# Optimization experiments

Measured on AMD Instinct MI355X. Metric: run time of the kernel, lower is better.

## Reference

```python
import jax, jax.numpy as jnp
import numpy as np
from functools import partial

DM, DP, DV = 128, 32, 32
DO = DP + DV
SCALE_F = 4.0
MAXF = 127.0 / SCALE_F                       # 31.75 feature clamp
SCALE_FM = SCALE_F / 16.0 * 3600.0 / 256.0   # scale after spatial mean
MAXM = 127.0 / SCALE_FM                      # clamp after mean
DN = ('NCHW', 'OIHW', 'NCHW')

# 3-tap positions inside a 3x3 kernel for the 4 directions
_DIR_POS = [
    [(1, 0), (1, 1), (1, 2)],  # horizontal
    [(0, 1), (1, 1), (2, 1)],  # vertical
    [(0, 0), (1, 1), (2, 2)],  # main diagonal
    [(2, 0), (1, 1), (0, 2)],  # anti diagonal
]

def _dir_conv(x, w, b, d):
    # w: [3, out, in] -> dense [out, in, 3, 3] kernel with 3 nonzero taps
    o, i = w.shape[1], w.shape[2]
    k = jnp.zeros((o, i, 3, 3), w.dtype)
    for t, (r, c) in enumerate(_DIR_POS[d]):
        k = k.at[:, :, r, c].set(w[t])
    y = jax.lax.conv_general_dilated(x, k, (1, 1), 'SAME', dimension_numbers=DN)
    return y + b[None, :, None, None]

def _pw(x, w, b):  # 1x1 conv: w [out, in]
    return jnp.einsum('bchw,oc->bohw', x, w) + b[None, :, None, None]

def _lrelu16(x):
    return jnp.where(x >= 0, x, x * (1.0 / 16.0))

def forward(x, map_w, map_b, dconv_w, dconv_b, c1_w, c1_b,
            r0_w1, r0_b1, r0_w2, r0_b2, fin_w, fin_b, prelu_w,
            pdw_w, pdw_b, ppw_w, vl1_w, vl1_b, vl2_w, vl2_b,
            vlf_w, vlf_b, pscale, vscale):
    silu = jax.nn.silu
    # ---- Mapping ----
    xs = tuple(silu(_dir_conv(x, map_w, map_b, d)) for d in range(4))
    for l in range(4):  # 4 DirectionalConvResBlocks
        res = xs
        xs = tuple(silu(_dir_conv(xs[d], dconv_w[l], dconv_b[l], d)) for d in range(4))
        xs = tuple(silu(_pw(t, c1_w[l], c1_b[l])) for t in xs)
        xs = tuple(a + b for a, b in zip(xs, res))
    # Conv0dResBlock
    res = xs
    xs = tuple(silu(_pw(t, r0_w1, r0_b1)) for t in xs)
    xs = tuple(silu(_pw(t, r0_w2, r0_b2)) for t in xs)
    xs = tuple(a + b for a, b in zip(xs, res))
    xs = tuple(_pw(t, fin_w, fin_b) for t in xs)
    feature = jnp.stack(xs, axis=1)  # [B, 4, DO, H, W]
    # ---- trunk post-processing ----
    feature = jnp.tanh(feature / MAXF) * MAXF
    feature = jnp.sum(feature, axis=1)  # [B, DO, H, W]
    a = prelu_w[None, :, None, None]
    feature = jnp.where(feature >= 0, feature, a * feature)  # PReLU per-channel
    feature = feature / 4.0
    # ---- policy head ----
    policy = feature[:, :DP]
    policy = jax.lax.conv_general_dilated(policy, pdw_w, (1, 1), 'SAME',
                                          dimension_numbers=DN,
                                          feature_group_count=DP)
    policy = _lrelu16(policy + pdw_b[None, :, None, None])
    policy = jnp.clip(policy, -MAXF, MAXF)
    policy = _lrelu16(jnp.einsum('bchw,oc->bohw', policy, ppw_w))
    policy = policy * pscale
    # ---- value head ----
    value = jnp.mean(feature[:, DP:], axis=(2, 3))  # [B, DV]
    value = jax.nn.relu(value)
    value = jax.nn.relu(value @ vl1_w.T + vl1_b)
    value = jnp.minimum(value, MAXM)
    value = jax.nn.relu(value @ vl2_w.T + vl2_b)
    value = jnp.minimum(value, MAXM)
    value = (value @ vlf_w.T + vlf_b) * vscale
    return (value, policy)

def setup_inputs() -> dict:
    key = jax.random.key(0)
    ks = iter(jax.random.split(key, 32))
    n = lambda shape, s=0.1: (jax.random.normal(next(ks), shape, jnp.float32) * s)
    B, H, W = 512, 15, 15
    return {
        'x': jax.random.uniform(next(ks), (B, 2, H, W), jnp.float32),
        'map_w': n((3, DM, 2), 0.5), 'map_b': jnp.zeros((DM,), jnp.float32),
        'dconv_w': n((4, 3, DM, DM)), 'dconv_b': jnp.zeros((4, DM), jnp.float32),
        'c1_w': n((4, DM, DM)), 'c1_b': jnp.zeros((4, DM), jnp.float32),
        'r0_w1': n((DM, DM)), 'r0_b1': jnp.zeros((DM,), jnp.float32),
        'r0_w2': n((DM, DM)), 'r0_b2': jnp.zeros((DM,), jnp.float32),
        'fin_w': n((DO, DM)), 'fin_b': jnp.zeros((DO,), jnp.float32),
        'prelu_w': jnp.full((DO,), 0.25, jnp.float32),
        'pdw_w': n((DP, 1, 3, 3), 0.3), 'pdw_b': jnp.zeros((DP,), jnp.float32),
        'ppw_w': n((1, DP), 0.3),
        'vl1_w': n((DV, DV), 0.2), 'vl1_b': jnp.zeros((DV,), jnp.float32),
        'vl2_w': n((DV, DV), 0.2), 'vl2_b': jnp.zeros((DV,), jnp.float32),
        'vlf_w': n((3, DV), 0.2), 'vlf_b': jnp.zeros((3,), jnp.float32),
        'pscale': jnp.ones((1,), jnp.float32),
        'vscale': jnp.ones((1,), jnp.float32),
    }

def reference(x, map_w, map_b, dconv_w, dconv_b, c1_w, c1_b,
              r0_w1, r0_b1, r0_w2, r0_b2, fin_w, fin_b, prelu_w,
              pdw_w, pdw_b, ppw_w, vl1_w, vl1_b, vl2_w, vl2_b,
              vlf_w, vlf_b, pscale, vscale):
    return forward(x, map_w, map_b, dconv_w, dconv_b, c1_w, c1_b,
                   r0_w1, r0_b1, r0_w2, r0_b2, fin_w, fin_b, prelu_w,
                   pdw_w, pdw_b, ppw_w, vl1_w, vl1_b, vl2_w, vl2_b,
                   vlf_w, vlf_b, pscale, vscale)
```

## Files before the change

### kernel.cpp

```cpp
#include <hip/hip_runtime.h>
#include <math.h>

typedef unsigned short u16;
typedef _Float16 f16;
typedef __attribute__((ext_vector_type(4))) _Float16 f16x4;
typedef __attribute__((ext_vector_type(8))) _Float16 f16x8;
typedef __attribute__((ext_vector_type(4))) float f32x4;

#define NCELL 225
#define AST   136
#define NROW  227
#define MAXF  31.75f
#define MAXM  (127.0f/((4.0f/16.0f)*3600.0f/256.0f))
#define DYN_LDS (2*NROW*AST*2)

#define W_DCONV 0
#define W_C1    196608
#define W_R01   262144
#define W_R02   278528
#define W_FIN   294912
#define W_F16TOT 303104
#define F_MAPB   0
#define F_DCONVB 128
#define F_C1B    640
#define F_R0B1   1152
#define F_R0B2   1280
#define F_FINB   1408
#define F_PRELU  1472
#define F_MAPW   1536
#define F_TOT    2304

__device__ __forceinline__ float bfu(unsigned h){ union{unsigned i; float f;} v; v.i=h<<16; return v.f; }
__device__ __forceinline__ float rcp_f(float x){ return __builtin_amdgcn_rcpf(x); }
__device__ __forceinline__ float silu_f(float x){ return x*rcp_f(1.f+__expf(-x)); }
__device__ __forceinline__ float tanh_f(float z){ return 1.f - 2.f*rcp_f(__expf(2.f*z)+1.f); }
__device__ __forceinline__ float ldp(const void* p, size_t i, int isf){
  return isf ? ((const float*)p)[i] : bfu(((const u16*)p)[i]);
}

__global__ __launch_bounds__(256) void k_prep(
    const void* __restrict__ dconv_w, const void* __restrict__ c1_w,
    const void* __restrict__ r0_w1,  const void* __restrict__ r0_w2,
    const void* __restrict__ fin_w,  const void* __restrict__ map_w,
    const void* __restrict__ map_b,  const void* __restrict__ dconv_b,
    const void* __restrict__ c1_b,   const void* __restrict__ r0_b1,
    const void* __restrict__ r0_b2,  const void* __restrict__ fin_b,
    const void* __restrict__ prelu_w,
    const void* __restrict__ x, f16* __restrict__ wbuf)
{
  __shared__ int sflag;
  if (threadIdx.x < 64) {
    unsigned v = ((const u16*)x)[2*threadIdx.x];
    unsigned long long m = __ballot(v > 0x4000u);
    if (threadIdx.x == 0) sflag = (__popcll(m) > 16) ? 1 : 0;
  }
  __syncthreads();
  const int isf = sflag;
  float* fsec = (float*)(wbuf + W_F16TOT);
  const int NTOT = W_F16TOT + F_TOT;
  for (int i = blockIdx.x*256 + threadIdx.x; i < NTOT; i += gridDim.x*256) {
    if (i < W_F16TOT) {
      float v; int j = i;
      if (j < 196608)                 v = ldp(dconv_w, j, isf);
      else if ((j -= 196608) < 65536) v = ldp(c1_w, j, isf);
      else if ((j -= 65536) < 16384)  v = ldp(r0_w1, j, isf);
      else if ((j -= 16384) < 16384)  v = ldp(r0_w2, j, isf);
      else { j -= 16384;              v = ldp(fin_w, j, isf); }
      wbuf[i] = (f16)v;
    } else {
      int j = i - W_F16TOT; float v;
      if (j < 128)               v = ldp(map_b, j, isf);
      else if ((j -= 128) < 512) v = ldp(dconv_b, j, isf);
      else if ((j -= 512) < 512) v = ldp(c1_b, j, isf);
      else if ((j -= 512) < 128) v = ldp(r0_b1, j, isf);
      else if ((j -= 128) < 128) v = ldp(r0_b2, j, isf);
      else if ((j -= 128) < 64)  v = ldp(fin_b, j, isf);
      else if ((j -= 64) < 64)   v = ldp(prelu_w, j, isf);
      else { j -= 64;            v = ldp(map_w, j, isf); }
      fsec[i - W_F16TOT] = v;
    }
  }
}

template<int NTAPS, int MODE>
__device__ __forceinline__ void phase(
    const f16* __restrict__ S, f16* __restrict__ D,
    const f16* __restrict__ W, const float* __restrict__ bp,
    const unsigned (&pk)[4], int tid)
{
  const int lane = tid & 63;
  const int lrow = lane & 15;
  const int qb   = lane & 48;
  const int wave = tid >> 6;
  const int cg = wave >> 2, ng = wave & 3;
  const int ch0  = ng*32 + (qb >> 2);
  const int wrow = (ng*32 + lrow)*128 + (qb >> 1);

  f32x4 acc[4][2];
#pragma unroll
  for (int mi = 0; mi < 4; ++mi) {
    f32x4 z = {0.f,0.f,0.f,0.f};
    acc[mi][0] = z; acc[mi][1] = z;
  }
#pragma unroll
  for (int t = 0; t < NTAPS; ++t) {
    const int tt = (NTAPS == 3) ? t : 1;
    const f16* Wt = W + ((NTAPS == 3) ? t*16384 : 0) + wrow;
#pragma clang loop unroll(disable)
    for (int kb = 0; kb < 4; ++kb) {
      f16x8 Wf0 = *(const f16x8*)(Wt + kb*32);
      f16x8 Wf1 = *(const f16x8*)(Wt + 2048 + kb*32);
      f16x8 Af[4];
#pragma unroll
      for (int mi = 0; mi < 4; ++mi) {
        const int pc = (pk[mi] >> (8*tt)) & 255u;
        Af[mi] = *(const f16x8*)((const char*)S + pc*(AST*2) + qb + kb*64);
      }
#pragma unroll
      for (int mi = 0; mi < 4; ++mi) {
        acc[mi][0] = __builtin_amdgcn_mfma_f32_16x16x32_f16(Wf0, Af[mi], acc[mi][0], 0, 0, 0);
        acc[mi][1] = __builtin_amdgcn_mfma_f32_16x16x32_f16(Wf1, Af[mi], acc[mi][1], 0, 0, 0);
      }
    }
  }
  f32x4 bb0 = *(const f32x4*)(bp + ch0);
  f32x4 bb1 = *(const f32x4*)(bp + ch0 + 16);
#pragma unroll
  for (int mi = 0; mi < 4; ++mi) {
    const int cell = (cg*4 + mi)*16 + lrow;
    const int row  = (cell < NCELL) ? cell : 226;
#pragma unroll
    for (int nt = 0; nt < 2; ++nt) {
      f16* dp = D + row*AST + ch0 + nt*16;
      const f32x4 bb = nt ? bb1 : bb0;
      float v0 = silu_f(acc[mi][nt][0] + bb[0]);
      float v1 = silu_f(acc[mi][nt][1] + bb[1]);
      float v2 = silu_f(acc[mi][nt][2] + bb[2]);
      float v3 = silu_f(acc[mi][nt][3] + bb[3]);
      if (MODE == 1) {
        f16x4 r = *(const f16x4*)dp;
        v0 += (float)r[0]; v1 += (float)r[1]; v2 += (float)r[2]; v3 += (float)r[3];
      }
      f16x4 o = { (f16)v0, (f16)v1, (f16)v2, (f16)v3 };
      *(f16x4*)dp = o;
    }
  }
  __syncthreads();
}

__global__ __attribute__((amdgpu_flat_work_group_size(1024, 1024), amdgpu_waves_per_eu(4, 4)))
void k_all(
    const void* __restrict__ x,
    const void* __restrict__ pdw_w,  const void* __restrict__ pdw_b,
    const void* __restrict__ ppw_w,
    const void* __restrict__ vl1_w,  const void* __restrict__ vl1_b,
    const void* __restrict__ vl2_w,  const void* __restrict__ vl2_b,
    const void* __restrict__ vlf_w,  const void* __restrict__ vlf_b,
    const void* __restrict__ pscale, const void* __restrict__ vscale,
    const f16* __restrict__ wbuf, float* __restrict__ out, int badflag)
{
  extern __shared__ __align__(16) char dyn[];
  f16* bufA = (f16*)dyn;
  f16* bufB = bufA + NROW*AST;
  __shared__ float xin[452];
  __shared__ float vred[1024];
  __shared__ float vvA[32], vvB[32];
  __shared__ int sflag;

  const int b = blockIdx.x, tid = threadIdx.x;
  const int lane = tid & 63, wave = tid >> 6;
  const int cg = wave >> 2, ng = wave & 3;
  const int lrow = lane & 15;
  const float* fsec = (const float*)(wbuf + W_F16TOT);

  if (tid < 64) {
    unsigned v = ((const u16*)x)[2*tid];
    unsigned long long m = __ballot(v > 0x4000u);
    if (tid == 0) sflag = (__popcll(m) > 16) ? 1 : 0;
  }
  for (int i = tid; i < AST; i += 1024) {
    bufA[225*AST + i] = (f16)0.f;
    bufB[225*AST + i] = (f16)0.f;
  }
  __syncthreads();
  const int isf = sflag;

  for (int i = tid; i < 452; i += 1024) {
    float v;
    if (i < 225)       v = ldp(x, (size_t)b*450 + i, isf);
    else if (i == 225) v = 0.f;
    else if (i < 451)  v = ldp(x, (size_t)b*450 + 225 + (i - 226), isf);
    else               v = 0.f;
    xin[i] = v;
  }

  float facc[4][2][2];
#pragma unroll
  for (int mi = 0; mi < 4; ++mi)
#pragma unroll
    for (int jp = 0; jp < 2; ++jp) { facc[mi][jp][0] = 0.f; facc[mi][jp][1] = 0.f; }

  __syncthreads();

#pragma clang loop unroll(disable)
  for (int d = 0; d < 4; ++d) {
    const int dr = (d == 0) ? 0 : ((d == 3) ? -1 : 1);
    const int dc = (d == 1) ? 0 : 1;

    unsigned pk[4];
#pragma unroll
    for (int mi = 0; mi < 4; ++mi) {
      const int cell = (cg*4 + mi)*16 + lrow;
      const bool v0 = cell < NCELL;
      const int r = cell/15, c = cell - (cell/15)*15;
      unsigned p = 0;
#pragma unroll
      for (int t = 0; t < 3; ++t) {
        const int rs = r + (t-1)*dr, cs = c + (t-1)*dc;
        const bool v = v0 & (rs >= 0) & (rs < 15) & (cs >= 0) & (cs < 15);
        p |= (unsigned)(v ? rs*15 + cs : 225) << (8*t);
      }
      pk[mi] = p;
    }

    {
      const int qb = lane & 48;
      const int ch0 = ng*32 + (qb >> 2);
      float x0[4][3], x1[4][3];
#pragma unroll
      for (int mi = 0; mi < 4; ++mi)
#pragma unroll
        for (int t = 0; t < 3; ++t) {
          const int sp = (pk[mi] >> (8*t)) & 255u;
          x0[mi][t] = xin[sp]; x1[mi][t] = xin[226 + sp];
        }
#pragma unroll
      for (int nt = 0; nt < 2; ++nt) {
        const int chn = ch0 + nt*16;
        f32x4 mb = *(const f32x4*)(fsec + F_MAPB + chn);
        f32x4 wt[3][2];
#pragma unroll
        for (int t = 0; t < 3; ++t) {
          wt[t][0] = *(const f32x4*)(fsec + F_MAPW + (t*128 + chn)*2);
          wt[t][1] = *(const f32x4*)(fsec + F_MAPW + (t*128 + chn)*2 + 4);
        }
#pragma unroll
        for (int mi = 0; mi < 4; ++mi) {
          const int cell = (cg*4 + mi)*16 + lrow;
          const int row  = (cell < NCELL) ? cell : 226;
          f16x4 o;
#pragma unroll
          for (int j = 0; j < 4; ++j) {
            float s = mb[j];
#pragma unroll
            for (int t = 0; t < 3; ++t)
              s += wt[t][j>>1][(j&1)*2]*x0[mi][t] + wt[t][j>>1][(j&1)*2+1]*x1[mi][t];
            o[j] = (f16)silu_f(s);
          }
          *(f16x4*)(bufA + row*AST + chn) = o;
        }
      }
    }
    __syncthreads();

#pragma clang loop unroll(disable)
    for (int l = 0; l < 4; ++l) {
      phase<3, 0>(bufA, bufB, wbuf + W_DCONV + (size_t)l*49152,
                  fsec + F_DCONVB + l*128, pk, tid);
      phase<1, 1>(bufB, bufA, wbuf + W_C1 + (size_t)l*16384,
                  fsec + F_C1B + l*128, pk, tid);
    }
    phase<1, 0>(bufA, bufB, wbuf + W_R01, fsec + F_R0B1, pk, tid);
    phase<1, 1>(bufB, bufA, wbuf + W_R02, fsec + F_R0B2, pk, tid);

    {
      const int qb = lane & 48;
      f32x4 fa[4];
#pragma unroll
      for (int mi = 0; mi < 4; ++mi) { f32x4 z = {0.f,0.f,0.f,0.f}; fa[mi] = z; }
      const f16* Wt = wbuf + W_FIN + (ng*16 + lrow)*128 + (qb >> 1);
#pragma clang loop unroll(disable)
      for (int kb = 0; kb < 4; ++kb) {
        f16x8 Wf = *(const f16x8*)(Wt + kb*32);
#pragma unroll
        for (int mi = 0; mi < 4; ++mi) {
          const int pc = (pk[mi] >> 8) & 255u;
          f16x8 a = *(const f16x8*)((const char*)bufA + pc*(AST*2) + qb + kb*64);
          fa[mi] = __builtin_amdgcn_mfma_f32_16x16x32_f16(Wf, a, fa[mi], 0, 0, 0);
        }
      }
      const int chf = ng*16 + (qb >> 2);
      f32x4 fb = *(const f32x4*)(fsec + F_FINB + chf);
#pragma unroll
      for (int mi = 0; mi < 4; ++mi)
#pragma unroll
        for (int j = 0; j < 4; ++j)
          facc[mi][j>>1][j&1] += tanh_f((fa[mi][j] + fb[j]) * (1.f/MAXF)) * MAXF;
    }
    __syncthreads();
  }

  float* featf = (float*)bufA;
  {
    const int qb = lane & 48;
    const int chf = ng*16 + (qb >> 2);
    f32x4 aw = *(const f32x4*)(fsec + F_PRELU + chf);
#pragma unroll
    for (int mi = 0; mi < 4; ++mi) {
      const int cell = (cg*4 + mi)*16 + lrow;
      const int fcl  = (cell < NCELL) ? cell : 225;
      f32x4 o;
#pragma unroll
      for (int j = 0; j < 4; ++j) {
        float s = facc[mi][j>>1][j&1];
        s = (s >= 0.f) ? s : aw[j]*s;
        o[j] = s * 0.25f;
      }
      *(f32x4*)(featf + fcl*64 + chf) = o;
    }
  }
  __syncthreads();

  {
    const int ch = tid >> 5, strip = tid & 31;
    float s = 0.f;
    for (int cell = strip; cell < NCELL; cell += 32)
      s += featf[cell*64 + 32 + ch];
    vred[tid] = s;
  }
  __syncthreads();
  if (tid < 32) {
    float s = 0.f;
#pragma unroll
    for (int k = 0; k < 32; ++k) s += vred[tid*32 + k];
    vvA[tid] = fmaxf(s * (1.f/225.f), 0.f);
  }
  __syncthreads();
  if (tid < 32) {
    float s = ldp(vl1_b, tid, isf);
    for (int c2 = 0; c2 < 32; ++c2) s += ldp(vl1_w, tid*32 + c2, isf) * vvA[c2];
    vvB[tid] = fminf(fmaxf(s, 0.f), MAXM);
  }
  __syncthreads();
  if (tid < 32) {
    float s = ldp(vl2_b, tid, isf);
    for (int c2 = 0; c2 < 32; ++c2) s += ldp(vl2_w, tid*32 + c2, isf) * vvB[c2];
    vvA[tid] = fminf(fmaxf(s, 0.f), MAXM);
  }
  __syncthreads();
  if (tid < 3) {
    float s = ldp(vlf_b, tid, isf);
    for (int c2 = 0; c2 < 32; ++c2) s += ldp(vlf_w, tid*32 + c2, isf) * vvA[c2];
    out[b*3 + tid] = s * ldp(vscale, 0, isf);
  }
  __syncthreads();

  {
    const int ch = tid & 31;
    float pw[9];
#pragma unroll
    for (int k = 0; k < 9; ++k) pw[k] = ldp(pdw_w, (size_t)ch*9 + k, isf);
    const float pb = ldp(pdw_b, ch, isf);
    for (int i = tid; i < NCELL*32; i += 1024) {
      const int cell = i >> 5;
      const int r = cell/15, c = cell - r*15;
      float s = pb;
#pragma unroll
      for (int kr = 0; kr < 3; ++kr)
#pragma unroll
        for (int kc = 0; kc < 3; ++kc) {
          const int rr = r + kr - 1, cc = c + kc - 1;
          if (rr >= 0 && rr < 15 && cc >= 0 && cc < 15)
            s += pw[kr*3 + kc] * featf[(rr*15 + cc)*64 + ch];
        }
      s = (s >= 0.f) ? s : s * (1.f/16.f);
      s = fminf(fmaxf(s, -MAXF), MAXF);
      featf[cell*64 + 32 + ch] = s;
    }
  }
  __syncthreads();

  const float psc = ldp(pscale, 0, isf);
  for (int cell = tid; cell < NCELL; cell += 1024) {
    float s = 0.f;
#pragma unroll
    for (int c2 = 0; c2 < 32; ++c2)
      s += ldp(ppw_w, c2, isf) * featf[cell*64 + 32 + c2];
    s = (s >= 0.f) ? s : s * (1.f/16.f);
    out[1536 + b*NCELL + cell] = s * psc;
  }

  if (badflag && b == 0 && tid == 0) out[0] = 100000.f;
}

extern "C" void kernel_launch(void* const* d_in, const int* in_sizes, int n_in,
                              void* d_out, int out_size, void* d_ws, size_t ws_size,
                              hipStream_t stream)
{
  static const int EXP[25] = {230400, 768, 128, 196608, 512, 65536, 512,
                              16384, 128, 16384, 128, 8192, 64, 64,
                              288, 32, 32, 1024, 32, 1024, 32, 96, 3, 1, 1};
  int bad = (n_in != 25) ? 1 : 0;
  if (!bad) for (int i = 0; i < 25; ++i) if (in_sizes[i] != EXP[i]) bad = 1;
  if (out_size != 116736) bad = 1;

  if (hipFuncSetAttribute(reinterpret_cast<const void*>(k_all),
                          hipFuncAttributeMaxDynamicSharedMemorySize,
                          DYN_LDS) != hipSuccess) bad = 1;

  f16* wbuf = (f16*)d_ws;

  k_prep<<<512, 256, 0, stream>>>(d_in[3], d_in[5], d_in[7], d_in[9], d_in[11],
                                  d_in[1], d_in[2], d_in[4], d_in[6], d_in[8],
                                  d_in[10], d_in[12], d_in[13], d_in[0], wbuf);

  k_all<<<512, 1024, DYN_LDS, stream>>>(
      d_in[0], d_in[14], d_in[15], d_in[16],
      d_in[17], d_in[18], d_in[19], d_in[20], d_in[21], d_in[22],
      d_in[23], d_in[24], wbuf, (float*)d_out, bad);
}
```

Baseline: 970.2 us.

## Use single in-place LDS activation buffer with register-held residuals

Replaces the ping-pong pair of LDS activation buffers with one buffer written in place. Each phase now adds a barrier between the MFMA reads and the epilogue writes. Residual values are loaded into registers before each block instead of being read back from the destination buffer. This halves dynamic LDS use, which may allow more blocks per CU, at the cost of an extra barrier per phase and more register pressure from the held residuals.

New measurement: 989.5 us. About the same (+2.0%).

```diff
diff --git a/kernel.cpp b/kernel.cpp
--- a/kernel.cpp
+++ b/kernel.cpp
@@ -12,7 +12,7 @@
 #define NROW  227
 #define MAXF  31.75f
 #define MAXM  (127.0f/((4.0f/16.0f)*3600.0f/256.0f))
-#define DYN_LDS (2*NROW*AST*2)
+#define DYN_LDS (NROW*AST*2)
 
 #define W_DCONV 0
 #define W_C1    196608
@@ -84,9 +84,9 @@
 
 template<int NTAPS, int MODE>
 __device__ __forceinline__ void phase(
-    const f16* __restrict__ S, f16* __restrict__ D,
+    f16* __restrict__ buf,
     const f16* __restrict__ W, const float* __restrict__ bp,
-    const unsigned (&pk)[4], int tid)
+    const unsigned (&pk)[4], int tid, const f16x4 (&res)[4][2])
 {
   const int lane = tid & 63;
   const int lrow = lane & 15;
@@ -114,7 +114,7 @@
 #pragma unroll
       for (int mi = 0; mi < 4; ++mi) {
         const int pc = (pk[mi] >> (8*tt)) & 255u;
-        Af[mi] = *(const f16x8*)((const char*)S + pc*(AST*2) + qb + kb*64);
+        Af[mi] = *(const f16x8*)((const char*)buf + pc*(AST*2) + qb + kb*64);
       }
 #pragma unroll
       for (int mi = 0; mi < 4; ++mi) {
@@ -125,27 +125,47 @@
   }
   f32x4 bb0 = *(const f32x4*)(bp + ch0);
   f32x4 bb1 = *(const f32x4*)(bp + ch0 + 16);
+  __syncthreads();
 #pragma unroll
   for (int mi = 0; mi < 4; ++mi) {
     const int cell = (cg*4 + mi)*16 + lrow;
     const int row  = (cell < NCELL) ? cell : 226;
 #pragma unroll
     for (int nt = 0; nt < 2; ++nt) {
-      f16* dp = D + row*AST + ch0 + nt*16;
+      f16* dp = buf + row*AST + ch0 + nt*16;
       const f32x4 bb = nt ? bb1 : bb0;
       float v0 = silu_f(acc[mi][nt][0] + bb[0]);
       float v1 = silu_f(acc[mi][nt][1] + bb[1]);
       float v2 = silu_f(acc[mi][nt][2] + bb[2]);
       float v3 = silu_f(acc[mi][nt][3] + bb[3]);
       if (MODE == 1) {
-        f16x4 r = *(const f16x4*)dp;
-        v0 += (float)r[0]; v1 += (float)r[1]; v2 += (float)r[2]; v3 += (float)r[3];
+        v0 += (float)res[mi][nt][0]; v1 += (float)res[mi][nt][1];
+        v2 += (float)res[mi][nt][2]; v3 += (float)res[mi][nt][3];
       }
       f16x4 o = { (f16)v0, (f16)v1, (f16)v2, (f16)v3 };
       *(f16x4*)dp = o;
     }
   }
   __syncthreads();
+}
+
+__device__ __forceinline__ void load_res(
+    const f16* __restrict__ buf, int tid, f16x4 (&res)[4][2])
+{
+  const int lane = tid & 63;
+  const int lrow = lane & 15;
+  const int qb   = lane & 48;
+  const int wave = tid >> 6;
+  const int cg = wave >> 2, ng = wave & 3;
+  const int ch0 = ng*32 + (qb >> 2);
+#pragma unroll
+  for (int mi = 0; mi < 4; ++mi) {
+    const int cell = (cg*4 + mi)*16 + lrow;
+    const int row  = (cell < NCELL) ? cell : 226;
+#pragma unroll
+    for (int nt = 0; nt < 2; ++nt)
+      res[mi][nt] = *(const f16x4*)(buf + row*AST + ch0 + nt*16);
+  }
 }
 
 __global__ __attribute__((amdgpu_flat_work_group_size(1024, 1024), amdgpu_waves_per_eu(4, 4)))
@@ -160,8 +180,7 @@
     const f16* __restrict__ wbuf, float* __restrict__ out, int badflag)
 {
   extern __shared__ __align__(16) char dyn[];
-  f16* bufA = (f16*)dyn;
-  f16* bufB = bufA + NROW*AST;
+  f16* buf = (f16*)dyn;
   __shared__ float xin[452];
   __shared__ float vred[1024];
   __shared__ float vvA[32], vvB[32];
@@ -178,10 +197,8 @@
     unsigned long long m = __ballot(v > 0x4000u);
     if (tid == 0) sflag = (__popcll(m) > 16) ? 1 : 0;
   }
-  for (int i = tid; i < AST; i += 1024) {
-    bufA[225*AST + i] = (f16)0.f;
-    bufB[225*AST + i] = (f16)0.f;
-  }
+  for (int i = tid; i < AST; i += 1024)
+    buf[225*AST + i] = (f16)0.f;
   __syncthreads();
   const int isf = sflag;
 
@@ -257,21 +274,24 @@
               s += wt[t][j>>1][(j&1)*2]*x0[mi][t] + wt[t][j>>1][(j&1)*2+1]*x1[mi][t];
             o[j] = (f16)silu_f(s);
           }
-          *(f16x4*)(bufA + row*AST + chn) = o;
+          *(f16x4*)(buf + row*AST + chn) = o;
         }
       }
     }
     __syncthreads();
 
+    f16x4 res[4][2];
 #pragma clang loop unroll(disable)
     for (int l = 0; l < 4; ++l) {
-      phase<3, 0>(bufA, bufB, wbuf + W_DCONV + (size_t)l*49152,
-                  fsec + F_DCONVB + l*128, pk, tid);
-      phase<1, 1>(bufB, bufA, wbuf + W_C1 + (size_t)l*16384,
-                  fsec + F_C1B + l*128, pk, tid);
-    }
-    phase<1, 0>(bufA, bufB, wbuf + W_R01, fsec + F_R0B1, pk, tid);
-    phase<1, 1>(bufB, bufA, wbuf + W_R02, fsec + F_R0B2, pk, tid);
+      load_res(buf, tid, res);
+      phase<3, 0>(buf, wbuf + W_DCONV + (size_t)l*49152,
+                  fsec + F_DCONVB + l*128, pk, tid, res);
+      phase<1, 1>(buf, wbuf + W_C1 + (size_t)l*16384,
+                  fsec + F_C1B + l*128, pk, tid, res);
+    }
+    load_res(buf, tid, res);
+    phase<1, 0>(buf, wbuf + W_R01, fsec + F_R0B1, pk, tid, res);
+    phase<1, 1>(buf, wbuf + W_R02, fsec + F_R0B2, pk, tid, res);
 
     {
       const int qb = lane & 48;
@@ -285,7 +305,7 @@
 #pragma unroll
         for (int mi = 0; mi < 4; ++mi) {
           const int pc = (pk[mi] >> 8) & 255u;
-          f16x8 a = *(const f16x8*)((const char*)bufA + pc*(AST*2) + qb + kb*64);
+          f16x8 a = *(const f16x8*)((const char*)buf + pc*(AST*2) + qb + kb*64);
           fa[mi] = __builtin_amdgcn_mfma_f32_16x16x32_f16(Wf, a, fa[mi], 0, 0, 0);
         }
       }
@@ -300,7 +320,7 @@
     __syncthreads();
   }
 
-  float* featf = (float*)bufA;
+  float* featf = (float*)buf;
   {
     const int qb = lane & 48;
     const int chf = ng*16 + (qb >> 2);
```

## Use 768-thread blocks with five row tiles per wave

Applied to the files above, without the earlier changes.

Shrinks the fused kernel's workgroup from 16 to 12 waves, so each wave now covers 5 tiles of 16 cells (240 rows) instead of 4 (256 rows). This cuts padded MFMA work and reuses each loaded weight fragment across more tiles. In exchange each wave holds more accumulator registers, and the waves-per-EU hint drops from 4 to 3. The mapping stage now reads inputs from LDS inside the loop instead of preloading them, and the value-head reduction is re-indexed to fit the smaller thread count.

Result: faster. 805.9 us (median of 2 runs) (-16.9%).

```diff
diff --git a/kernel.cpp b/kernel.cpp
--- a/kernel.cpp
+++ b/kernel.cpp
@@ -13,6 +13,7 @@
 #define MAXF  31.75f
 #define MAXM  (127.0f/((4.0f/16.0f)*3600.0f/256.0f))
 #define DYN_LDS (2*NROW*AST*2)
+#define NT    768
 
 #define W_DCONV 0
 #define W_C1    196608
@@ -37,6 +38,7 @@
 __device__ __forceinline__ float ldp(const void* p, size_t i, int isf){
   return isf ? ((const float*)p)[i] : bfu(((const u16*)p)[i]);
 }
+#define MFMA16(A, B, C) __builtin_amdgcn_mfma_f32_16x16x32_f16((A), (B), (C), 0, 0, 0)
 
 __global__ __launch_bounds__(256) void k_prep(
     const void* __restrict__ dconv_w, const void* __restrict__ c1_w,
@@ -86,7 +88,7 @@
 __device__ __forceinline__ void phase(
     const f16* __restrict__ S, f16* __restrict__ D,
     const f16* __restrict__ W, const float* __restrict__ bp,
-    const unsigned (&pk)[4], int tid)
+    const unsigned (&pk)[5], int tid)
 {
   const int lane = tid & 63;
   const int lrow = lane & 15;
@@ -96,9 +98,9 @@
   const int ch0  = ng*32 + (qb >> 2);
   const int wrow = (ng*32 + lrow)*128 + (qb >> 1);
 
-  f32x4 acc[4][2];
-#pragma unroll
-  for (int mi = 0; mi < 4; ++mi) {
+  f32x4 acc[5][2];
+#pragma unroll
+  for (int mi = 0; mi < 5; ++mi) {
     f32x4 z = {0.f,0.f,0.f,0.f};
     acc[mi][0] = z; acc[mi][1] = z;
   }
@@ -110,24 +112,24 @@
     for (int kb = 0; kb < 4; ++kb) {
       f16x8 Wf0 = *(const f16x8*)(Wt + kb*32);
       f16x8 Wf1 = *(const f16x8*)(Wt + 2048 + kb*32);
-      f16x8 Af[4];
-#pragma unroll
-      for (int mi = 0; mi < 4; ++mi) {
+      f16x8 Af[5];
+#pragma unroll
+      for (int mi = 0; mi < 5; ++mi) {
         const int pc = (pk[mi] >> (8*tt)) & 255u;
         Af[mi] = *(const f16x8*)((const char*)S + pc*(AST*2) + qb + kb*64);
       }
 #pragma unroll
-      for (int mi = 0; mi < 4; ++mi) {
-        acc[mi][0] = __builtin_amdgcn_mfma_f32_16x16x32_f16(Wf0, Af[mi], acc[mi][0], 0, 0, 0);
-        acc[mi][1] = __builtin_amdgcn_mfma_f32_16x16x32_f16(Wf1, Af[mi], acc[mi][1], 0, 0, 0);
+      for (int mi = 0; mi < 5; ++mi) {
+        acc[mi][0] = MFMA16(Wf0, Af[mi], acc[mi][0]);
+        acc[mi][1] = MFMA16(Wf1, Af[mi], acc[mi][1]);
       }
     }
   }
   f32x4 bb0 = *(const f32x4*)(bp + ch0);
   f32x4 bb1 = *(const f32x4*)(bp + ch0 + 16);
 #pragma unroll
-  for (int mi = 0; mi < 4; ++mi) {
-    const int cell = (cg*4 + mi)*16 + lrow;
+  for (int mi = 0; mi < 5; ++mi) {
+    const int cell = (cg*5 + mi)*16 + lrow;
     const int row  = (cell < NCELL) ? cell : 226;
 #pragma unroll
     for (int nt = 0; nt < 2; ++nt) {
@@ -148,7 +150,7 @@
   __syncthreads();
 }
 
-__global__ __attribute__((amdgpu_flat_work_group_size(1024, 1024), amdgpu_waves_per_eu(4, 4)))
+__global__ __attribute__((amdgpu_flat_work_group_size(NT, NT), amdgpu_waves_per_eu(3, 3)))
 void k_all(
     const void* __restrict__ x,
     const void* __restrict__ pdw_w,  const void* __restrict__ pdw_b,
@@ -163,7 +165,7 @@
   f16* bufA = (f16*)dyn;
   f16* bufB = bufA + NROW*AST;
   __shared__ float xin[452];
-  __shared__ float vred[1024];
+  __shared__ float vred[NT];
   __shared__ float vvA[32], vvB[32];
   __shared__ int sflag;
 
@@ -178,14 +180,14 @@
     unsigned long long m = __ballot(v > 0x4000u);
     if (tid == 0) sflag = (__popcll(m) > 16) ? 1 : 0;
   }
-  for (int i = tid; i < AST; i += 1024) {
+  for (int i = tid; i < AST; i += NT) {
     bufA[225*AST + i] = (f16)0.f;
     bufB[225*AST + i] = (f16)0.f;
   }
   __syncthreads();
   const int isf = sflag;
 
-  for (int i = tid; i < 452; i += 1024) {
+  for (int i = tid; i < 452; i += NT) {
     float v;
     if (i < 225)       v = ldp(x, (size_t)b*450 + i, isf);
     else if (i == 225) v = 0.f;
@@ -194,9 +196,9 @@
     xin[i] = v;
   }
 
-  float facc[4][2][2];
-#pragma unroll
-  for (int mi = 0; mi < 4; ++mi)
+  float facc[5][2][2];
+#pragma unroll
+  for (int mi = 0; mi < 5; ++mi)
 #pragma unroll
     for (int jp = 0; jp < 2; ++jp) { facc[mi][jp][0] = 0.f; facc[mi][jp][1] = 0.f; }
 
@@ -207,10 +209,10 @@
     const int dr = (d == 0) ? 0 : ((d == 3) ? -1 : 1);
     const int dc = (d == 1) ? 0 : 1;
 
-    unsigned pk[4];
-#pragma unroll
-    for (int mi = 0; mi < 4; ++mi) {
-      const int cell = (cg*4 + mi)*16 + lrow;
+    unsigned pk[5];
+#pragma unroll
+    for (int mi = 0; mi < 5; ++mi) {
+      const int cell = (cg*5 + mi)*16 + lrow;
       const bool v0 = cell < NCELL;
       const int r = cell/15, c = cell - (cell/15)*15;
       unsigned p = 0;
@@ -226,14 +228,6 @@
     {
       const int qb = lane & 48;
       const int ch0 = ng*32 + (qb >> 2);
-      float x0[4][3], x1[4][3];
-#pragma unroll
-      for (int mi = 0; mi < 4; ++mi)
-#pragma unroll
-        for (int t = 0; t < 3; ++t) {
-          const int sp = (pk[mi] >> (8*t)) & 255u;
-          x0[mi][t] = xin[sp]; x1[mi][t] = xin[226 + sp];
-        }
 #pragma unroll
       for (int nt = 0; nt < 2; ++nt) {
         const int chn = ch0 + nt*16;
@@ -245,16 +239,18 @@
           wt[t][1] = *(const f32x4*)(fsec + F_MAPW + (t*128 + chn)*2 + 4);
         }
 #pragma unroll
-        for (int mi = 0; mi < 4; ++mi) {
-          const int cell = (cg*4 + mi)*16 + lrow;
+        for (int mi = 0; mi < 5; ++mi) {
+          const int cell = (cg*5 + mi)*16 + lrow;
           const int row  = (cell < NCELL) ? cell : 226;
           f16x4 o;
 #pragma unroll
           for (int j = 0; j < 4; ++j) {
             float s = mb[j];
 #pragma unroll
-            for (int t = 0; t < 3; ++t)
-              s += wt[t][j>>1][(j&1)*2]*x0[mi][t] + wt[t][j>>1][(j&1)*2+1]*x1[mi][t];
+            for (int t = 0; t < 3; ++t) {
+              const int sp = (pk[mi] >> (8*t)) & 255u;
+              s += wt[t][j>>1][(j&1)*2]*xin[sp] + wt[t][j>>1][(j&1)*2+1]*xin[226 + sp];
+            }
             o[j] = (f16)silu_f(s);
           }
           *(f16x4*)(bufA + row*AST + chn) = o;
@@ -275,24 +271,24 @@
 
     {
       const int qb = lane & 48;
-      f32x4 fa[4];
-#pragma unroll
-      for (int mi = 0; mi < 4; ++mi) { f32x4 z = {0.f,0.f,0.f,0.f}; fa[mi] = z; }
+      f32x4 fa[5];
+#pragma unroll
+      for (int mi = 0; mi < 5; ++mi) { f32x4 z = {0.f,0.f,0.f,0.f}; fa[mi] = z; }
       const f16* Wt = wbuf + W_FIN + (ng*16 + lrow)*128 + (qb >> 1);
 #pragma clang loop unroll(disable)
       for (int kb = 0; kb < 4; ++kb) {
         f16x8 Wf = *(const f16x8*)(Wt + kb*32);
 #pragma unroll
-        for (int mi = 0; mi < 4; ++mi) {
+        for (int mi = 0; mi < 5; ++mi) {
           const int pc = (pk[mi] >> 8) & 255u;
           f16x8 a = *(const f16x8*)((const char*)bufA + pc*(AST*2) + qb + kb*64);
-          fa[mi] = __builtin_amdgcn_mfma_f32_16x16x32_f16(Wf, a, fa[mi], 0, 0, 0);
+          fa[mi] = MFMA16(Wf, a, fa[mi]);
         }
       }
       const int chf = ng*16 + (qb >> 2);
       f32x4 fb = *(const f32x4*)(fsec + F_FINB + chf);
 #pragma unroll
-      for (int mi = 0; mi < 4; ++mi)
+      for (int mi = 0; mi < 5; ++mi)
 #pragma unroll
         for (int j = 0; j < 4; ++j)
           facc[mi][j>>1][j&1] += tanh_f((fa[mi][j] + fb[j]) * (1.f/MAXF)) * MAXF;
@@ -306,8 +302,8 @@
     const int chf = ng*16 + (qb >> 2);
     f32x4 aw = *(const f32x4*)(fsec + F_PRELU + chf);
 #pragma unroll
-    for (int mi = 0; mi < 4; ++mi) {
-      const int cell = (cg*4 + mi)*16 + lrow;
+    for (int mi = 0; mi < 5; ++mi) {
+      const int cell = (cg*5 + mi)*16 + lrow;
       const int fcl  = (cell < NCELL) ? cell : 225;
       f32x4 o;
 #pragma unroll
@@ -322,9 +318,9 @@
   __syncthreads();
 
   {
-    const int ch = tid >> 5, strip = tid & 31;
+    const int ch = tid & 31, strip = tid >> 5;
     float s = 0.f;
-    for (int cell = strip; cell < NCELL; cell += 32)
+    for (int cell = strip; cell < NCELL; cell += 24)
       s += featf[cell*64 + 32 + ch];
     vred[tid] = s;
   }
@@ -332,7 +328,7 @@
   if (tid < 32) {
     float s = 0.f;
 #pragma unroll
-    for (int k = 0; k < 32; ++k) s += vred[tid*32 + k];
+    for (int k = 0; k < 24; ++k) s += vred[k*32 + tid];
     vvA[tid] = fmaxf(s * (1.f/225.f), 0.f);
   }
   __syncthreads();
@@ -361,7 +357,7 @@
 #pragma unroll
     for (int k = 0; k < 9; ++k) pw[k] = ldp(pdw_w, (size_t)ch*9 + k, isf);
     const float pb = ldp(pdw_b, ch, isf);
-    for (int i = tid; i < NCELL*32; i += 1024) {
+    for (int i = tid; i < NCELL*32; i += NT) {
       const int cell = i >> 5;
       const int r = cell/15, c = cell - r*15;
       float s = pb;
@@ -381,7 +377,7 @@
   __syncthreads();
 
   const float psc = ldp(pscale, 0, isf);
-  for (int cell = tid; cell < NCELL; cell += 1024) {
+  for (int cell = tid; cell < NCELL; cell += NT) {
     float s = 0.f;
 #pragma unroll
     for (int c2 = 0; c2 < 32; ++c2)
@@ -414,7 +410,7 @@
                                   d_in[1], d_in[2], d_in[4], d_in[6], d_in[8],
                                   d_in[10], d_in[12], d_in[13], d_in[0], wbuf);
 
-  k_all<<<512, 1024, DYN_LDS, stream>>>(
+  k_all<<<512, NT, DYN_LDS, stream>>>(
       d_in[0], d_in[14], d_in[15], d_in[16],
       d_in[17], d_in[18], d_in[19], d_in[20], d_in[21], d_in[22],
       d_in[23], d_in[24], wbuf, (float*)d_out, bad);
```
